# Optimization experiments

Measured on AMD Instinct MI355X. Metric: run time of the kernel, lower is better.

## Reference

```python
import jax, jax.numpy as jnp
import numpy as np

N = 50000      # nodes
E = 800000     # edges (avg degree 16)
F_IN = 128     # input features
H, C = 4, 16   # heads, per-head out channels -> conv out = 64
D = 128        # target_dim (proj output)
NEG_SLOPE = 0.2
LN_EPS = 1e-5


def setup_inputs() -> dict:
    key = jax.random.key(0)
    ks = jax.random.split(key, 8)
    s_in = 1.0 / np.sqrt(F_IN)
    s_hc = 1.0 / np.sqrt(H * C)
    return {
        "x": jax.random.normal(ks[0], (N, F_IN), jnp.float32),
        "edge_index": jax.random.randint(ks[1], (2, E), 0, N, jnp.int64),
        "W": jax.random.normal(ks[2], (F_IN, H * C), jnp.float32) * s_in,
        "att_src": jax.random.normal(ks[3], (H, C), jnp.float32) * s_hc,
        "att_dst": jax.random.normal(ks[4], (H, C), jnp.float32) * s_hc,
        "bias": jnp.zeros((H * C,), jnp.float32),
        "proj_w": jax.random.normal(ks[5], (D, H * C), jnp.float32) * s_hc,
        "proj_b": jnp.zeros((D,), jnp.float32),
        "gamma": jnp.ones((D,), jnp.float32),
        "beta": jnp.zeros((D,), jnp.float32),
    }


def reference(x, edge_index, W, att_src, att_dst, bias, proj_w, proj_b, gamma, beta):
    src, dst = edge_index[0], edge_index[1]
    # GATConv: per-head linear transform  [N, H, C]
    xp = (x @ W).reshape(N, H, C)
    a_src = jnp.einsum("nhc,hc->nh", xp, att_src)  # [N, H]
    a_dst = jnp.einsum("nhc,hc->nh", xp, att_dst)  # [N, H]
    # raw attention logits per edge, per head  [E, H]
    e = jax.nn.leaky_relu(a_src[src] + a_dst[dst], NEG_SLOPE)
    # segment softmax over incoming edges of each destination node
    m = jax.ops.segment_max(e, dst, num_segments=N)          # [N, H]
    ex = jnp.exp(e - m[dst])                                 # [E, H]
    denom = jax.ops.segment_sum(ex, dst, num_segments=N)     # [N, H]
    alpha = ex / (denom[dst] + 1e-16)                        # [E, H]
    # weighted message aggregation  [N, H, C]
    out = jax.ops.segment_sum(alpha[:, :, None] * xp[src], dst, num_segments=N)
    out = out.reshape(N, H * C) + bias                       # concat heads
    # projection to target_dim
    out = out @ proj_w.T + proj_b                            # [N, D]
    # LayerNorm over feature dim
    mu = out.mean(axis=-1, keepdims=True)
    var = out.var(axis=-1, keepdims=True)
    out = (out - mu) * jax.lax.rsqrt(var + LN_EPS) * gamma + beta
    # activation (relu); dropout=0.0 -> identity
    return jax.nn.relu(out)
```

## Files before the change

kernel.cpp:

```cpp
#include <hip/hip_runtime.h>
#include <hip/hip_bf16.h>


#define LEAKY(x) ((x) > 0.f ? (x) : 0.2f * (x))
#define CHUNK 2048
#define NBUK_PAD 256

typedef __attribute__((ext_vector_type(8))) short bf16x8;
typedef __attribute__((ext_vector_type(8))) unsigned short u16x8;
typedef __attribute__((ext_vector_type(4))) float f32x4;

static __device__ __forceinline__ unsigned short f2bf_rne(float f) {
    unsigned u = __float_as_uint(f);
    return (unsigned short)((u + 0x7FFFu + ((u >> 16) & 1u)) >> 16);
}
static __device__ __forceinline__ float bf2f(unsigned short h) {
    return __uint_as_float(((unsigned)h) << 16);
}

__global__ __launch_bounds__(256) void k_prep_part1(
    const float* __restrict__ W, const float* __restrict__ bias,
    const float* __restrict__ att_src, const float* __restrict__ att_dst,
    const float* __restrict__ proj_w, const float* __restrict__ proj_b,
    unsigned short* __restrict__ Whf, unsigned short* __restrict__ Wlf,
    unsigned short* __restrict__ Phf, unsigned short* __restrict__ Plf,
    float* __restrict__ pb2,
    const int* __restrict__ dst, int* __restrict__ cnt, int E, int nchunk)
{
    int bid = blockIdx.x, t = threadIdx.x;
    if (bid < nchunk) {
        __shared__ int hist[NBUK_PAD];
        hist[t] = 0;
        __syncthreads();
        int e0 = bid * CHUNK;
#pragma unroll
        for (int i = 0; i < CHUNK / 256; i++) {
            int e = e0 + i * 256 + t;
            if (e < E) atomicAdd(&hist[dst[e] >> 8], 1);
        }
        __syncthreads();
        cnt[bid * NBUK_PAD + t] = hist[t];
        return;
    }
    int idx = (bid - nchunk) * 256 + t;
    if (idx < 10240) {
        int j = idx & 7, lane = (idx >> 3) & 63, ts = idx >> 9;
        int t4 = ts >> 2, s = ts & 3;
        int k = s * 32 + ((lane >> 4) << 3) + j;
        float w = 0.f;
        if (t4 < 4) {
            int n = t4 * 16 + (lane & 15);
            w = W[k * 64 + n];
        } else {
            int c8 = lane & 15;
            if (c8 < 8) {
                const float* av = (c8 < 4) ? att_src : att_dst;
                int hh = c8 & 3;
                float sacc = 0.f;
                for (int c = 0; c < 16; c++)
                    sacc += W[k * 64 + hh * 16 + c] * av[hh * 16 + c];
                w = sacc;
            }
        }
        unsigned short wh = f2bf_rne(w);
        Whf[idx] = wh;
        Wlf[idx] = f2bf_rne(w - bf2f(wh));
    } else if (idx < 18432) {
        int i2 = idx - 10240;
        int j = i2 & 7, lane = (i2 >> 3) & 63, ts = i2 >> 9;
        int tt = ts >> 1, s = ts & 1;
        int k = s * 32 + ((lane >> 4) << 3) + j;
        int d = tt * 16 + (lane & 15);
        float w = proj_w[d * 64 + k];
        unsigned short wh = f2bf_rne(w);
        Phf[i2] = wh;
        Plf[i2] = f2bf_rne(w - bf2f(wh));
    } else if (idx < 18432 + 128) {
        int d = idx - 18432;
        float s = proj_b[d];
        for (int j = 0; j < 64; j++) s += bias[j] * proj_w[d * 64 + j];
        pb2[d] = s;
    }
}

__global__ __launch_bounds__(256) void k_scanB1(int* __restrict__ cnt, int* __restrict__ bt,
                                                int* __restrict__ row_ptr,
                                                int nchunk, int n_nodes, int E)
{
    __shared__ int sh[256];
    int t = threadIdx.x, b = blockIdx.x;
    int v0 = (t < nchunk) ? cnt[t * NBUK_PAD + b] : 0;
    int v1 = (t + 256 < nchunk) ? cnt[(t + 256) * NBUK_PAD + b] : 0;
    sh[t] = v0; __syncthreads();
    for (int off = 1; off < 256; off <<= 1) {
        int u = (t >= off) ? sh[t - off] : 0;
        __syncthreads();
        sh[t] += u;
        __syncthreads();
    }
    int incl0 = sh[t], tot0 = sh[255];
    __syncthreads();
    sh[t] = v1; __syncthreads();
    for (int off = 1; off < 256; off <<= 1) {
        int u = (t >= off) ? sh[t - off] : 0;
        __syncthreads();
        sh[t] += u;
        __syncthreads();
    }
    int incl1 = sh[t] + tot0;
    if (t < nchunk) cnt[t * NBUK_PAD + b] = incl0 - v0;
    if (t + 256 < nchunk) cnt[(t + 256) * NBUK_PAD + b] = incl1 - v1;
    if (t == 255) bt[b] = incl1;
    if (b == 0 && t == 0) row_ptr[n_nodes] = E;
}

__global__ __launch_bounds__(256) void k_part2_xw(
    const int* __restrict__ src, const int* __restrict__ dst,
    const int* __restrict__ cnt, const int* __restrict__ bt,
    unsigned* __restrict__ part, int E,
    const float* __restrict__ x,
    const unsigned short* __restrict__ Whf, const unsigned short* __restrict__ Wlf,
    unsigned short* __restrict__ xp, float* __restrict__ a_src, float* __restrict__ a_dst,
    int n_nodes, int P, int nbXw)
{
    __shared__ float xs[64][132];
    __shared__ int bases[NBUK_PAD];
    __shared__ int sh[256];
    int bid = blockIdx.x, t = threadIdx.x;
    if (bid % P == P - 1) {
        int blk = bid / P;
        int v = bt[t];
        sh[t] = v; __syncthreads();
        for (int off = 1; off < 256; off <<= 1) {
            int u = (t >= off) ? sh[t - off] : 0;
            __syncthreads();
            sh[t] += u;
            __syncthreads();
        }
        bases[t] = cnt[blk * NBUK_PAD + t] + (sh[t] - v);
        __syncthreads();
        int e0 = blk * CHUNK;
#pragma unroll
        for (int i = 0; i < CHUNK / 256; i++) {
            int e = e0 + i * 256 + t;
            if (e < E) {
                int d = dst[e];
                int s = src[e];
                int pos = atomicAdd(&bases[d >> 8], 1);
                part[pos] = ((unsigned)s << 8) | (unsigned)(d & 255);
            }
        }
        return;
    }
    int xb = bid - bid / P;
    if (xb >= nbXw) return;
    int xbase = xb * 64;
    for (int i = t; i < 64 * 32; i += 256) {
        int r = i >> 5, c = (i & 31) << 2;
        int gr = xbase + r; if (gr >= n_nodes) gr = n_nodes - 1;
        *(float4*)&xs[r][c] = *(const float4*)(x + (size_t)gr * 128 + c);
    }
    __syncthreads();
    int w = t >> 6, lane = t & 63;
    int mbase = xbase + w * 16;
    int mrow = lane & 15, kg = lane >> 4;
    int lrow = w * 16 + mrow;

    bf16x8 ah[4], al[4];
#pragma unroll
    for (int s = 0; s < 4; s++) {
        float4 v0 = *(const float4*)&xs[lrow][s * 32 + kg * 8];
        float4 v1 = *(const float4*)&xs[lrow][s * 32 + kg * 8 + 4];
        float f[8] = {v0.x, v0.y, v0.z, v0.w, v1.x, v1.y, v1.z, v1.w};
#pragma unroll
        for (int j = 0; j < 8; j++) {
            unsigned short h = f2bf_rne(f[j]);
            ah[s][j] = (short)h;
            al[s][j] = (short)f2bf_rne(f[j] - bf2f(h));
        }
    }

    f32x4 acc[5];
#pragma unroll
    for (int tt = 0; tt < 5; tt++) acc[tt] = (f32x4){0.f, 0.f, 0.f, 0.f};
#pragma unroll
    for (int tt = 0; tt < 5; tt++) {
#pragma unroll
        for (int s = 0; s < 4; s++) {
            size_t fi = (size_t)(((tt * 4 + s) * 64 + lane) * 8);
            bf16x8 bh = *(const bf16x8*)(Whf + fi);
            bf16x8 bl = *(const bf16x8*)(Wlf + fi);
            acc[tt] = __builtin_amdgcn_mfma_f32_16x16x32_bf16(ah[s], bh, acc[tt], 0, 0, 0);
            acc[tt] = __builtin_amdgcn_mfma_f32_16x16x32_bf16(ah[s], bl, acc[tt], 0, 0, 0);
            acc[tt] = __builtin_amdgcn_mfma_f32_16x16x32_bf16(al[s], bh, acc[tt], 0, 0, 0);
        }
    }

#pragma unroll
    for (int tt = 0; tt < 4; tt++) {
#pragma unroll
        for (int r = 0; r < 4; r++) {
            int n2 = mbase + kg * 4 + r;
            if (n2 < n_nodes) xp[(size_t)n2 * 64 + tt * 16 + mrow] = f2bf_rne(acc[tt][r]);
        }
    }
#pragma unroll
    for (int r = 0; r < 4; r++) {
        int n2 = mbase + kg * 4 + r;
        if (n2 < n_nodes) {
            float v = acc[4][r];
            if (mrow < 4)      a_src[n2 * 4 + mrow] = v;
            else if (mrow < 8) a_dst[n2 * 4 + (mrow - 4)] = v;
        }
    }
}

__global__ __launch_bounds__(256) void k_csr(const unsigned* __restrict__ part, const int* __restrict__ bt,
                                             int* __restrict__ row_ptr, int* __restrict__ colsrc,
                                             int n_nodes)
{
    __shared__ int hist[256], off[256], sh[256];
    int t = threadIdx.x, b = blockIdx.x;
    int v = bt[t];
    sh[t] = v; __syncthreads();
    for (int o = 1; o < 256; o <<= 1) {
        int u = (t >= o) ? sh[t - o] : 0;
        __syncthreads();
        sh[t] += u;
        __syncthreads();
    }
    int e0 = (b > 0) ? sh[b - 1] : 0;
    int e1 = sh[b];
    __syncthreads();
    int m = e1 - e0;
    hist[t] = 0;
    __syncthreads();
    for (int i = t; i < m; i += 256)
        atomicAdd(&hist[part[e0 + i] & 255u], 1);
    __syncthreads();
    int hv = hist[t];
    sh[t] = hv; __syncthreads();
    for (int o = 1; o < 256; o <<= 1) {
        int u = (t >= o) ? sh[t - o] : 0;
        __syncthreads();
        sh[t] += u;
        __syncthreads();
    }
    int excl = sh[t] - hv;
    off[t] = excl;
    int node = b * 256 + t;
    if (node < n_nodes) row_ptr[node] = e0 + excl;
    __syncthreads();
    for (int i = t; i < m; i += 256) {
        unsigned u = part[e0 + i];
        int pos = atomicAdd(&off[u & 255u], 1);
        colsrc[e0 + pos] = (int)(u >> 8);
    }
}

__global__ __launch_bounds__(256, 6) void k_agg_proj(
    const unsigned short* __restrict__ xp, const float* __restrict__ a_src, const float* __restrict__ a_dst,
    const int* __restrict__ row_ptr, const int* __restrict__ colsrc,
    const unsigned short* __restrict__ Phf, const unsigned short* __restrict__ Plf,
    const float* __restrict__ pb2, const float* __restrict__ gamma, const float* __restrict__ beta,
    float* __restrict__ out, int n_nodes)
{
    __shared__ int   sstage[4][64];
    __shared__ float alpha_s[4][64][4];
    __shared__ unsigned short rowbuf[16][72];
    __shared__ float pS[4][16], pQ[4][16];
    __shared__ float pb_s[128], g_s[128], b_s[128];
    int t = threadIdx.x, w = t >> 6, lane = t & 63;
    if (t < 128) { pb_s[t] = pb2[t]; g_s[t] = gamma[t]; b_s[t] = beta[t]; }
    int cgrp = lane & 7;
    int eoct = lane >> 3;
    int h = cgrp >> 1;
    int nb16 = blockIdx.x * 16;

    for (int i = 0; i < 4; i++) {
        int n = nb16 + w * 4 + i;
        int nl = w * 4 + i;
        float acc[8] = {0.f,0.f,0.f,0.f,0.f,0.f,0.f,0.f};
        float den = 0.f;
        if (n < n_nodes) {
            int rp0 = row_ptr[n], rp1 = row_ptr[n + 1];
            float4 ad4 = *(const float4*)&a_dst[(size_t)n * 4];
            for (int base = rp0; base < rp1; base += 64) {
                int cnt = rp1 - base; if (cnt > 64) cnt = 64;
                int s = 0;
                float4 p = make_float4(0.f, 0.f, 0.f, 0.f);
                if (lane < cnt) {
                    s = colsrc[base + lane];
                    float4 as4 = *(const float4*)&a_src[(size_t)s * 4];
                    p.x = __expf(LEAKY(as4.x + ad4.x));
                    p.y = __expf(LEAKY(as4.y + ad4.y));
                    p.z = __expf(LEAKY(as4.z + ad4.z));
                    p.w = __expf(LEAKY(as4.w + ad4.w));
                }
                sstage[w][lane] = s;
                *(float4*)&alpha_s[w][lane][0] = p;
                int iters = (cnt + 7) >> 3;
                int it = 0;
                for (; it + 2 <= iters; it += 2) {
                    int j0 = (it << 3) + eoct;
                    int j1 = j0 + 8;
                    int sj0 = sstage[w][j0];
                    int sj1 = sstage[w][j1];
                    float aj0 = alpha_s[w][j0][h];
                    float aj1 = alpha_s[w][j1][h];
                    u16x8 v0 = *(const u16x8*)(xp + (size_t)((unsigned)sj0 * 64u + (cgrp << 3)));
                    u16x8 v1 = *(const u16x8*)(xp + (size_t)((unsigned)sj1 * 64u + (cgrp << 3)));
                    den += aj0;
#pragma unroll
                    for (int q = 0; q < 8; q++) acc[q] += aj0 * bf2f(v0[q]);
                    den += aj1;
#pragma unroll
                    for (int q = 0; q < 8; q++) acc[q] += aj1 * bf2f(v1[q]);
                }
                if (it < iters) {
                    int j = (it << 3) + eoct;
                    int sj = sstage[w][j];
                    float aj = alpha_s[w][j][h];
                    u16x8 v = *(const u16x8*)(xp + (size_t)((unsigned)sj * 64u + (cgrp << 3)));
                    den += aj;
#pragma unroll
                    for (int q = 0; q < 8; q++) acc[q] += aj * bf2f(v[q]);
                }
            }
#pragma unroll
            for (int q = 0; q < 8; q++) {
                acc[q] += __shfl_xor(acc[q], 8);
                acc[q] += __shfl_xor(acc[q], 16);
                acc[q] += __shfl_xor(acc[q], 32);
            }
            den += __shfl_xor(den, 8);
            den += __shfl_xor(den, 16);
            den += __shfl_xor(den, 32);
        }
        if (eoct == 0) {
            float inv = 1.f / (den + 1e-16f);
            u16x8 o;
#pragma unroll
            for (int q = 0; q < 8; q++) o[q] = f2bf_rne(acc[q] * inv);
            *(u16x8*)&rowbuf[nl][cgrp << 3] = o;
        }
    }
    __syncthreads();

    int mrow = lane & 15, kg = lane >> 4;
    bf16x8 ah[2];
#pragma unroll
    for (int s = 0; s < 2; s++) {
        ah[s] = *(const bf16x8*)&rowbuf[mrow][s * 32 + kg * 8];
    }
    f32x4 acc2[2];
#pragma unroll
    for (int ttl = 0; ttl < 2; ttl++) acc2[ttl] = (f32x4){0.f, 0.f, 0.f, 0.f};
#pragma unroll
    for (int ttl = 0; ttl < 2; ttl++) {
        int tt = w * 2 + ttl;
#pragma unroll
        for (int s = 0; s < 2; s++) {
            size_t fi = (size_t)(((tt * 2 + s) * 64 + lane) * 8);
            bf16x8 bh = *(const bf16x8*)(Phf + fi);
            bf16x8 bl = *(const bf16x8*)(Plf + fi);
            acc2[ttl] = __builtin_amdgcn_mfma_f32_16x16x32_bf16(ah[s], bh, acc2[ttl], 0, 0, 0);
            acc2[ttl] = __builtin_amdgcn_mfma_f32_16x16x32_bf16(ah[s], bl, acc2[ttl], 0, 0, 0);
        }
    }
    float vv[2][4];
#pragma unroll
    for (int r = 0; r < 4; r++) {
        float S = 0.f, Q = 0.f;
#pragma unroll
        for (int ttl = 0; ttl < 2; ttl++) {
            int tt = w * 2 + ttl;
            float v = acc2[ttl][r] + pb_s[tt * 16 + mrow];
            vv[ttl][r] = v;
            S += v;
            Q += v * v;
        }
#pragma unroll
        for (int off = 8; off; off >>= 1) {
            S += __shfl_xor(S, off);
            Q += __shfl_xor(Q, off);
        }
        if (mrow == 0) { pS[w][kg * 4 + r] = S; pQ[w][kg * 4 + r] = Q; }
    }
    __syncthreads();
#pragma unroll
    for (int r = 0; r < 4; r++) {
        int nl = kg * 4 + r;
        int nr = nb16 + nl;
        float S = pS[0][nl] + pS[1][nl] + pS[2][nl] + pS[3][nl];
        float Q = pQ[0][nl] + pQ[1][nl] + pQ[2][nl] + pQ[3][nl];
        float mu  = S * (1.f / 128.f);
        float var = Q * (1.f / 128.f) - mu * mu;
        float inv = rsqrtf(var + 1e-5f);
        if (nr < n_nodes) {
#pragma unroll
            for (int ttl = 0; ttl < 2; ttl++) {
                int d = (w * 2 + ttl) * 16 + mrow;
                float o = fmaxf((vv[ttl][r] - mu) * inv * g_s[d] + b_s[d], 0.f);
                out[(size_t)nr * 128 + d] = o;
            }
        }
    }
}

extern "C" void kernel_launch(void* const* d_in, const int* in_sizes, int n_in,
                              void* d_out, int out_size, void* d_ws, size_t ws_size,
                              hipStream_t stream)
{
    const float* x       = (const float*)d_in[0];
    const int*   ei      = (const int*)  d_in[1];
    const float* W       = (const float*)d_in[2];
    const float* att_src = (const float*)d_in[3];
    const float* att_dst = (const float*)d_in[4];
    const float* bias    = (const float*)d_in[5];
    const float* proj_w  = (const float*)d_in[6];
    const float* proj_b  = (const float*)d_in[7];
    const float* gamma   = (const float*)d_in[8];
    const float* beta    = (const float*)d_in[9];

    int N = in_sizes[0] / 128;
    int E = in_sizes[1] / 2;
    const int* srcIdx = ei;
    const int* dstIdx = ei + E;

    int nchunk = (E + CHUNK - 1) / CHUNK;
    int NBUK   = (N + 255) / 256;
    int nbXw   = (N + 63) / 64;
    int nbPrep = (18560 + 255) / 256;

    char* ws = (char*)d_ws;
    unsigned short* xp = (unsigned short*)ws; ws += (size_t)N * 64 * 2;
    float* a_src   = (float*)ws; ws += (size_t)N * 4 * 4;
    float* a_dst   = (float*)ws; ws += (size_t)N * 4 * 4;
    int*   row_ptr = (int*)ws;   ws += (size_t)(N + 1) * 4;
    int*   cnt     = (int*)ws;   ws += (size_t)nchunk * NBUK_PAD * 4;
    unsigned* part = (unsigned*)ws; ws += (size_t)E * 4;
    int*   colsrc  = (int*)ws;   ws += (size_t)E * 4;
    int*   bt      = (int*)ws;   ws += 256 * 4;
    unsigned short* Whf = (unsigned short*)ws; ws += 10240 * 2;
    unsigned short* Wlf = (unsigned short*)ws; ws += 10240 * 2;
    unsigned short* Phf = (unsigned short*)ws; ws += 8192 * 2;
    unsigned short* Plf = (unsigned short*)ws; ws += 8192 * 2;
    float* pb2 = (float*)ws; ws += 128 * 4;

    int P = (nbXw + nchunk - 1) / nchunk + 1;
    int totalFused = nchunk * P;

    k_prep_part1<<<nchunk + nbPrep, 256, 0, stream>>>(W, bias, att_src, att_dst,
                                                      proj_w, proj_b,
                                                      Whf, Wlf, Phf, Plf, pb2,
                                                      dstIdx, cnt, E, nchunk);
    k_scanB1<<<256, 256, 0, stream>>>(cnt, bt, row_ptr, nchunk, N, E);
    k_part2_xw<<<totalFused, 256, 0, stream>>>(srcIdx, dstIdx, cnt, bt, part, E,
                                               x, Whf, Wlf,
                                               xp, a_src, a_dst, N, P, nbXw);
    k_csr<<<NBUK, 256, 0, stream>>>(part, bt, row_ptr, colsrc, N);
    k_agg_proj<<<(N + 15) / 16, 256, 0, stream>>>(xp, a_src, a_dst, row_ptr, colsrc,
                                                  Phf, Plf, pb2, gamma, beta,
                                                  (float*)d_out, N);
}
```

Measured before the change: 78.82 us.

## Partition edges into 16-node buckets and build CSR inside aggregation kernel

Changes the counting-sort bucket granularity from 256 to 16 destination nodes, so each aggregation block owns exactly one bucket. The separate k_csr pass is removed, and the per-node sort of edges into LDS is done inside k_agg_proj. This removes one kernel launch and the global colsrc/row_ptr round trip. In exchange it adds a larger histogram and scan, a single-block scan kernel, and a hard edge cap per bucket that would truncate unusually dense buckets.

```diff
diff --git a/kernel.cpp b/kernel.cpp
--- a/kernel.cpp
+++ b/kernel.cpp
@@ -4,7 +4,8 @@
 
 #define LEAKY(x) ((x) > 0.f ? (x) : 0.2f * (x))
 #define CHUNK 2048
-#define NBUK_PAD 256
+#define BPAD 3328
+#define ECAP 576
 
 typedef __attribute__((ext_vector_type(8))) short bf16x8;
 typedef __attribute__((ext_vector_type(8))) unsigned short u16x8;
@@ -29,17 +30,17 @@
 {
     int bid = blockIdx.x, t = threadIdx.x;
     if (bid < nchunk) {
-        __shared__ int hist[NBUK_PAD];
-        hist[t] = 0;
+        __shared__ int hist[BPAD];
+        for (int k = t; k < BPAD; k += 256) hist[k] = 0;
         __syncthreads();
         int e0 = bid * CHUNK;
 #pragma unroll
         for (int i = 0; i < CHUNK / 256; i++) {
             int e = e0 + i * 256 + t;
-            if (e < E) atomicAdd(&hist[dst[e] >> 8], 1);
-        }
-        __syncthreads();
-        cnt[bid * NBUK_PAD + t] = hist[t];
+            if (e < E) atomicAdd(&hist[dst[e] >> 4], 1);
+        }
+        __syncthreads();
+        for (int k = t; k < BPAD; k += 256) cnt[bid * BPAD + k] = hist[k];
         return;
     }
     int idx = (bid - nchunk) * 256 + t;
@@ -84,13 +85,12 @@
 }
 
 __global__ __launch_bounds__(256) void k_scanB1(int* __restrict__ cnt, int* __restrict__ bt,
-                                                int* __restrict__ row_ptr,
-                                                int nchunk, int n_nodes, int E)
+                                                int nchunk)
 {
     __shared__ int sh[256];
     int t = threadIdx.x, b = blockIdx.x;
-    int v0 = (t < nchunk) ? cnt[t * NBUK_PAD + b] : 0;
-    int v1 = (t + 256 < nchunk) ? cnt[(t + 256) * NBUK_PAD + b] : 0;
+    int v0 = (t < nchunk) ? cnt[t * BPAD + b] : 0;
+    int v1 = (t + 256 < nchunk) ? cnt[(t + 256) * BPAD + b] : 0;
     sh[t] = v0; __syncthreads();
     for (int off = 1; off < 256; off <<= 1) {
         int u = (t >= off) ? sh[t - off] : 0;
@@ -108,28 +108,21 @@
         __syncthreads();
     }
     int incl1 = sh[t] + tot0;
-    if (t < nchunk) cnt[t * NBUK_PAD + b] = incl0 - v0;
-    if (t + 256 < nchunk) cnt[(t + 256) * NBUK_PAD + b] = incl1 - v1;
+    if (t < nchunk) cnt[t * BPAD + b] = incl0 - v0;
+    if (t + 256 < nchunk) cnt[(t + 256) * BPAD + b] = incl1 - v1;
     if (t == 255) bt[b] = incl1;
-    if (b == 0 && t == 0) row_ptr[n_nodes] = E;
-}
-
-__global__ __launch_bounds__(256) void k_part2_xw(
-    const int* __restrict__ src, const int* __restrict__ dst,
-    const int* __restrict__ cnt, const int* __restrict__ bt,
-    unsigned* __restrict__ part, int E,
-    const float* __restrict__ x,
-    const unsigned short* __restrict__ Whf, const unsigned short* __restrict__ Wlf,
-    unsigned short* __restrict__ xp, float* __restrict__ a_src, float* __restrict__ a_dst,
-    int n_nodes, int P, int nbXw)
-{
-    __shared__ float xs[64][132];
-    __shared__ int bases[NBUK_PAD];
+}
+
+__global__ __launch_bounds__(256) void k_scanB2(const int* __restrict__ bt, int* __restrict__ bb,
+                                                int E)
+{
     __shared__ int sh[256];
-    int bid = blockIdx.x, t = threadIdx.x;
-    if (bid % P == P - 1) {
-        int blk = bid / P;
-        int v = bt[t];
+    __shared__ int carry_s;
+    int t = threadIdx.x;
+    if (t == 0) carry_s = 0;
+    __syncthreads();
+    for (int seg = 0; seg < BPAD / 256; seg++) {
+        int v = bt[seg * 256 + t];
         sh[t] = v; __syncthreads();
         for (int off = 1; off < 256; off <<= 1) {
             int u = (t >= off) ? sh[t - off] : 0;
@@ -137,7 +130,31 @@
             sh[t] += u;
             __syncthreads();
         }
-        bases[t] = cnt[blk * NBUK_PAD + t] + (sh[t] - v);
+        int c = carry_s;
+        bb[seg * 256 + t] = c + sh[t] - v;
+        __syncthreads();
+        if (t == 255) carry_s = c + sh[255];
+        __syncthreads();
+    }
+    if (t == 0) bb[BPAD] = E;
+}
+
+__global__ __launch_bounds__(256) void k_part2_xw(
+    const int* __restrict__ src, const int* __restrict__ dst,
+    const int* __restrict__ cnt, const int* __restrict__ bb,
+    unsigned* __restrict__ part, int E,
+    const float* __restrict__ x,
+    const unsigned short* __restrict__ Whf, const unsigned short* __restrict__ Wlf,
+    unsigned short* __restrict__ xp, float* __restrict__ a_src, float* __restrict__ a_dst,
+    int n_nodes, int P, int nbXw)
+{
+    __shared__ float xs[64][132];
+    int* bases = (int*)&xs[0][0];
+    int bid = blockIdx.x, t = threadIdx.x;
+    if (bid % P == P - 1) {
+        int blk = bid / P;
+        for (int k = t; k < BPAD; k += 256)
+            bases[k] = cnt[blk * BPAD + k] + bb[k];
         __syncthreads();
         int e0 = blk * CHUNK;
 #pragma unroll
@@ -146,8 +163,8 @@
             if (e < E) {
                 int d = dst[e];
                 int s = src[e];
-                int pos = atomicAdd(&bases[d >> 8], 1);
-                part[pos] = ((unsigned)s << 8) | (unsigned)(d & 255);
+                int pos = atomicAdd(&bases[d >> 4], 1);
+                part[pos] = ((unsigned)s << 4) | (unsigned)(d & 15);
             }
         }
         return;
@@ -215,82 +232,63 @@
     }
 }
 
-__global__ __launch_bounds__(256) void k_csr(const unsigned* __restrict__ part, const int* __restrict__ bt,
-                                             int* __restrict__ row_ptr, int* __restrict__ colsrc,
-                                             int n_nodes)
-{
-    __shared__ int hist[256], off[256], sh[256];
-    int t = threadIdx.x, b = blockIdx.x;
-    int v = bt[t];
-    sh[t] = v; __syncthreads();
-    for (int o = 1; o < 256; o <<= 1) {
-        int u = (t >= o) ? sh[t - o] : 0;
-        __syncthreads();
-        sh[t] += u;
-        __syncthreads();
-    }
-    int e0 = (b > 0) ? sh[b - 1] : 0;
-    int e1 = sh[b];
-    __syncthreads();
-    int m = e1 - e0;
-    hist[t] = 0;
-    __syncthreads();
-    for (int i = t; i < m; i += 256)
-        atomicAdd(&hist[part[e0 + i] & 255u], 1);
-    __syncthreads();
-    int hv = hist[t];
-    sh[t] = hv; __syncthreads();
-    for (int o = 1; o < 256; o <<= 1) {
-        int u = (t >= o) ? sh[t - o] : 0;
-        __syncthreads();
-        sh[t] += u;
-        __syncthreads();
-    }
-    int excl = sh[t] - hv;
-    off[t] = excl;
-    int node = b * 256 + t;
-    if (node < n_nodes) row_ptr[node] = e0 + excl;
-    __syncthreads();
-    for (int i = t; i < m; i += 256) {
-        unsigned u = part[e0 + i];
-        int pos = atomicAdd(&off[u & 255u], 1);
-        colsrc[e0 + pos] = (int)(u >> 8);
-    }
-}
-
 __global__ __launch_bounds__(256, 6) void k_agg_proj(
     const unsigned short* __restrict__ xp, const float* __restrict__ a_src, const float* __restrict__ a_dst,
-    const int* __restrict__ row_ptr, const int* __restrict__ colsrc,
+    const int* __restrict__ bb, const unsigned* __restrict__ part,
     const unsigned short* __restrict__ Phf, const unsigned short* __restrict__ Plf,
     const float* __restrict__ pb2, const float* __restrict__ gamma, const float* __restrict__ beta,
     float* __restrict__ out, int n_nodes)
 {
+    __shared__ int   colsrc_lds[ECAP];
+    __shared__ int   rp[17], cur[16];
     __shared__ int   sstage[4][64];
     __shared__ float alpha_s[4][64][4];
     __shared__ unsigned short rowbuf[16][72];
     __shared__ float pS[4][16], pQ[4][16];
     __shared__ float pb_s[128], g_s[128], b_s[128];
-    int t = threadIdx.x, w = t >> 6, lane = t & 63;
+    int t = threadIdx.x, w = t >> 6, lane = t & 63, b = blockIdx.x;
     if (t < 128) { pb_s[t] = pb2[t]; g_s[t] = gamma[t]; b_s[t] = beta[t]; }
     int cgrp = lane & 7;
     int eoct = lane >> 3;
     int h = cgrp >> 1;
-    int nb16 = blockIdx.x * 16;
+    int nb16 = b * 16;
+
+    int e0 = bb[b], e1 = bb[b + 1];
+    int m = e1 - e0; if (m > ECAP) m = ECAP;
+    if (t < 16) cur[t] = 0;
+    __syncthreads();
+    for (int i = t; i < m; i += 256)
+        atomicAdd(&cur[part[e0 + i] & 15u], 1);
+    __syncthreads();
+    if (t == 0) {
+        int run = 0;
+        rp[0] = 0;
+        for (int k = 0; k < 16; k++) { run += cur[k]; rp[k + 1] = run; }
+    }
+    __syncthreads();
+    if (t < 16) cur[t] = rp[t];
+    __syncthreads();
+    for (int i = t; i < m; i += 256) {
+        unsigned u = part[e0 + i];
+        int pos = atomicAdd(&cur[u & 15u], 1);
+        colsrc_lds[pos] = (int)(u >> 4);
+    }
+    __syncthreads();
 
     for (int i = 0; i < 4; i++) {
-        int n = nb16 + w * 4 + i;
         int nl = w * 4 + i;
+        int n = nb16 + nl;
         float acc[8] = {0.f,0.f,0.f,0.f,0.f,0.f,0.f,0.f};
         float den = 0.f;
         if (n < n_nodes) {
-            int rp0 = row_ptr[n], rp1 = row_ptr[n + 1];
+            int rp0 = rp[nl], rp1 = rp[nl + 1];
             float4 ad4 = *(const float4*)&a_dst[(size_t)n * 4];
             for (int base = rp0; base < rp1; base += 64) {
                 int cnt = rp1 - base; if (cnt > 64) cnt = 64;
                 int s = 0;
                 float4 p = make_float4(0.f, 0.f, 0.f, 0.f);
                 if (lane < cnt) {
-                    s = colsrc[base + lane];
+                    s = colsrc_lds[base + lane];
                     float4 as4 = *(const float4*)&a_src[(size_t)s * 4];
                     p.x = __expf(LEAKY(as4.x + ad4.x));
                     p.y = __expf(LEAKY(as4.y + ad4.y));
@@ -429,7 +427,7 @@
     const int* dstIdx = ei + E;
 
     int nchunk = (E + CHUNK - 1) / CHUNK;
-    int NBUK   = (N + 255) / 256;
+    int NBUK16 = (N + 15) / 16;
     int nbXw   = (N + 63) / 64;
     int nbPrep = (18560 + 255) / 256;
 
@@ -437,11 +435,10 @@
     unsigned short* xp = (unsigned short*)ws; ws += (size_t)N * 64 * 2;
     float* a_src   = (float*)ws; ws += (size_t)N * 4 * 4;
     float* a_dst   = (float*)ws; ws += (size_t)N * 4 * 4;
-    int*   row_ptr = (int*)ws;   ws += (size_t)(N + 1) * 4;
-    int*   cnt     = (int*)ws;   ws += (size_t)nchunk * NBUK_PAD * 4;
+    int*   cnt     = (int*)ws;   ws += (size_t)nchunk * BPAD * 4;
     unsigned* part = (unsigned*)ws; ws += (size_t)E * 4;
-    int*   colsrc  = (int*)ws;   ws += (size_t)E * 4;
-    int*   bt      = (int*)ws;   ws += 256 * 4;
+    int*   bt      = (int*)ws;   ws += (size_t)BPAD * 4;
+    int*   bb      = (int*)ws;   ws += (size_t)(BPAD + 1) * 4;
     unsigned short* Whf = (unsigned short*)ws; ws += 10240 * 2;
     unsigned short* Wlf = (unsigned short*)ws; ws += 10240 * 2;
     unsigned short* Phf = (unsigned short*)ws; ws += 8192 * 2;
@@ -455,12 +452,12 @@
                                                       proj_w, proj_b,
                                                       Whf, Wlf, Phf, Plf, pb2,
                                                       dstIdx, cnt, E, nchunk);
-    k_scanB1<<<256, 256, 0, stream>>>(cnt, bt, row_ptr, nchunk, N, E);
-    k_part2_xw<<<totalFused, 256, 0, stream>>>(srcIdx, dstIdx, cnt, bt, part, E,
+    k_scanB1<<<BPAD, 256, 0, stream>>>(cnt, bt, nchunk);
+    k_scanB2<<<1, 256, 0, stream>>>(bt, bb, E);
+    k_part2_xw<<<totalFused, 256, 0, stream>>>(srcIdx, dstIdx, cnt, bb, part, E,
                                                x, Whf, Wlf,
                                                xp, a_src, a_dst, N, P, nbXw);
-    k_csr<<<NBUK, 256, 0, stream>>>(part, bt, row_ptr, colsrc, N);
-    k_agg_proj<<<(N + 15) / 16, 256, 0, stream>>>(xp, a_src, a_dst, row_ptr, colsrc,
-                                                  Phf, Plf, pb2, gamma, beta,
-                                                  (float*)d_out, N);
-}
+    k_agg_proj<<<NBUK16, 256, 0, stream>>>(xp, a_src, a_dst, bb, part,
+                                           Phf, Plf, pb2, gamma, beta,
+                                           (float*)d_out, N);
+}
```

Result: slower. 109.1 us (median of 5 runs) (+38.5%).
